# Kernel tuning notes

Hardware: AMD Instinct MI355X
Metric: run time of the kernel (lower is better)

Reference implementation:

```python
import jax, jax.numpy as jnp
import numpy as np

B, N, K = 4096, 64, 4


def _jump_sum(Ls, rho):
    # sum_k L_k @ rho @ L_k^dagger  (real dtype -> dagger == transpose)
    return jnp.einsum('kij,bjl,kml->bim', Ls, rho, Ls)


def _sandwich(U, rho):
    # U @ rho @ U^dagger
    return jnp.einsum('ij,bjl,ml->bim', U, rho, U)


def setup_inputs() -> dict:
    key = jax.random.key(0)
    k = jax.random.split(key, 6)
    eye = jnp.eye(N, dtype=jnp.float32)
    rho0 = jax.random.normal(k[0], (B, N, N), dtype=jnp.float32)
    # propagators: near-identity perturbations, Um well-conditioned for the LU solve
    U1 = eye + 0.1 * jax.random.normal(k[1], (N, N), dtype=jnp.float32)
    Um = eye + 0.1 * jax.random.normal(k[2], (N, N), dtype=jnp.float32)
    Ls0 = jax.random.normal(k[3], (K, N, N), dtype=jnp.float32)
    Lsmid = jax.random.normal(k[4], (K, N, N), dtype=jnp.float32)
    Ls1 = jax.random.normal(k[5], (K, N, N), dtype=jnp.float32)
    dt = jnp.asarray(0.01, dtype=jnp.float32)
    return {'rho0': rho0, 'U1': U1, 'Um': Um, 'Ls0': Ls0,
            'Lsmid': Lsmid, 'Ls1': Ls1, 'dt': dt}


def reference(rho0, U1, Um, Ls0, Lsmid, Ls1, dt):
    # propagator from t+dt/2 to t+dt via LU solve: solve(Um^T, U1^T)^T
    Um1 = jnp.linalg.solve(Um.T, U1.T).T

    # stage 1
    rho1 = rho0
    # stage 2 (SecondStage, no_jump_0 = Um, Ls = Ls0, aii = 0.5)
    rho2 = _sandwich(Um, rho0 + 0.5 * dt * _jump_sum(Ls0, rho1))
    # stage 3 (SameTimeStage, no_jump_0 = Um, Ls = Lsmid, aii = 0.5)
    rho3 = _sandwich(Um, rho0) + 0.5 * dt * _jump_sum(Lsmid, rho2)
    rho23 = rho2 + rho3
    # stage 4 (RKStage, no_jump_0 = U1, no_jump_i = Um1, Ls = Lsmid, aii = 1.0)
    rho4 = _sandwich(U1, rho0) + _sandwich(Um1, dt * _jump_sum(Lsmid, rho3))

    out = (_sandwich(U1, rho0 + (dt / 6) * _jump_sum(Ls0, rho1))
           + _sandwich(Um1, (dt / 3) * _jump_sum(Lsmid, rho23))
           + (dt / 6) * _jump_sum(Ls1, rho4))
    return out
```

## Files before the change

kernel.cpp:

```cpp
#include <hip/hip_runtime.h>


typedef __attribute__((ext_vector_type(16))) float f32x16;
typedef __attribute__((ext_vector_type(8))) __bf16 bf16x8;

#define MATB 8192

__device__ __forceinline__ unsigned short bf16rne(float x) {
  unsigned u = __builtin_bit_cast(unsigned, x);
  return (unsigned short)((u + 0x7FFFu + ((u >> 16) & 1u)) >> 16);
}
__device__ __forceinline__ float bflo(unsigned u) {
  return __builtin_bit_cast(float, u << 16);
}
__device__ __forceinline__ float bfhi(unsigned u) {
  return __builtin_bit_cast(float, u & 0xFFFF0000u);
}
__device__ __forceinline__ unsigned pk2(float lo, float hi) {
  union { __bf16 h[2]; unsigned u; } r;
  r.h[0] = (__bf16)lo;
  r.h[1] = (__bf16)hi;
  return r.u;
}

union U4 { uint4 u; bf16x8 h; };

__device__ __forceinline__ bf16x8 assemble(const f32x16& t, int b8, int lh) {
  unsigned u0 = pk2(t[b8 + 0], t[b8 + 1]);
  unsigned u1 = pk2(t[b8 + 2], t[b8 + 3]);
  unsigned w0 = pk2(t[b8 + 4], t[b8 + 5]);
  unsigned w1 = pk2(t[b8 + 6], t[b8 + 7]);
  unsigned z0 = lh ? u0 : w0;
  unsigned z1 = lh ? u1 : w1;
  unsigned r0 = __shfl_xor(z0, 32);
  unsigned r1 = __shfl_xor(z1, 32);
  U4 r;
  r.u = make_uint4(lh ? r0 : u0, lh ? r1 : u1,
                   lh ? w0 : r0, lh ? w1 : r1);
  return r.h;
}

__global__ __launch_bounds__(256) void kraus_invert(
    const float* __restrict__ U1, const float* __restrict__ Um,
    float* __restrict__ Um1) {
  __shared__ float M[64][66];
  __shared__ float X[64][66];
  int tid = threadIdx.x;
#pragma unroll
  for (int it = 0; it < 16; ++it) {
    int idx = tid + 256 * it;
    int r = idx >> 6, c = idx & 63;
    M[r][c] = Um[idx];
    X[r][c] = (r == c) ? 1.0f : 0.0f;
  }
  __syncthreads();
  for (int k = 0; k < 64; ++k) {
    if (tid < 64) {
      float ip = 1.0f / M[k][k];
      M[k][tid] *= ip;
      X[k][tid] *= ip;
    }
    __syncthreads();
    int r = tid & 63, q = tid >> 6;
    float f = M[r][k];
    __syncthreads();
    if (r != k) {
#pragma unroll
      for (int cc = 0; cc < 16; ++cc) {
        int c = q * 16 + cc;
        M[r][c] -= f * M[k][c];
        X[r][c] -= f * X[k][c];
      }
    }
    __syncthreads();
  }
  for (int it = 0; it < 16; ++it) {
    int idx = tid + 256 * it;
    int i = idx >> 6, j = idx & 63;
    float s = 0.0f;
#pragma unroll 4
    for (int k = 0; k < 64; ++k) s += U1[i * 64 + k] * X[k][j];
    Um1[idx] = s;
  }
}

__global__ __launch_bounds__(256) void kraus_prepack(
    const float* __restrict__ U1, const float* __restrict__ Um,
    const float* __restrict__ Ls0, const float* __restrict__ Lsmid,
    const float* __restrict__ Ls1, float* __restrict__ ws) {
  const float* Um1 = ws;
  unsigned short* dst = (unsigned short*)((char*)ws + 16384);
  int o = blockIdx.x;
  const float* s;
  if (o == 0) s = U1;
  else if (o == 1) s = Um;
  else if (o == 2) s = Um1;
  else if (o < 7) s = Ls0 + (o - 3) * 4096;
  else if (o < 11) s = Lsmid + (o - 7) * 4096;
  else s = Ls1 + (o - 11) * 4096;
  unsigned short* d = dst + o * 4096;
  int tid = threadIdx.x;
#pragma unroll
  for (int j = 0; j < 16; ++j) {
    int idx = tid + 256 * j;
    int f = idx >> 9, l = (idx >> 3) & 63, i = idx & 7;
    int t = f >> 2, ss = f & 3;
    int R = t * 32 + (l & 31);
    int C = ss * 16 + (l >> 5) * 8 + i;
    d[idx] = bf16rne(s[R * 64 + C]);
  }
}

__global__ __launch_bounds__(256, 4) void kraus_main(
    const float* __restrict__ rho0g, const float* __restrict__ dtp,
    const char* __restrict__ gfrag, float* __restrict__ outg) {
  __shared__ __align__(16) char lds[5 * MATB];
  char* S0 = lds;
  char* S1 = S0 + MATB;
  char* S2 = S1 + MATB;
  char* S3 = S2 + MATB;
  char* S4 = S3 + MATB;

  const int tid = threadIdx.x;
  const int l = tid & 63, w = tid >> 6;
  const int ti = w >> 1, tj = w & 1;
  const int l31 = l & 31, lh = l >> 5;
  const int fragoff = l * 16;
  const int myslot = ((tj * 4 + 2 * ti) << 10) + fragoff;
  const float dt = dtp[0];
  const size_t b = blockIdx.x;

  auto GF = [&](int op, int blk) {
    return gfrag + op * 8192 + blk * 4096 + l * 16;
  };
  auto mmA = [&](f32x16& acc, const char* X, int a, const char* __restrict__ gQ) {
#pragma unroll
    for (int s = 0; s < 4; ++s) {
      bf16x8 aa = *(const bf16x8*)(X + ((a * 4 + s) << 10) + fragoff);
      bf16x8 bb = *(const bf16x8*)(gQ + s * 1024);
      acc = __builtin_amdgcn_mfma_f32_32x32x16_bf16(aa, bb, acc, 0, 0, 0);
    }
  };
  auto sandP = [&](f32x16& acc, const char* X, int op1, int op2) {
    f32x16 t0 = {}, t1 = {};
    mmA(t0, X, 0, GF(op1, ti));
    mmA(t1, X, 1, GF(op1, ti));
    const char* gQ = GF(op2, tj);
#pragma unroll
    for (int s = 0; s < 4; ++s) {
      bf16x8 p = assemble((s < 2) ? t0 : t1, (s & 1) * 8, lh);
      bf16x8 q = *(const bf16x8*)(gQ + s * 1024);
      acc = __builtin_amdgcn_mfma_f32_32x32x16_bf16(p, q, acc, 0, 0, 0);
    }
  };
  auto storeF = [&](char* dst, const f32x16& acc) {
#pragma unroll
    for (int sg = 0; sg < 2; ++sg) {
      bf16x8 f = assemble(acc, sg * 8, lh);
      *(bf16x8*)(dst + myslot + (sg << 10)) = f;
    }
  };
  auto axpy = [&](char* D, const char* A, float s, const char* Bm) {
#pragma unroll
    for (int j = 0; j < 8; ++j) {
      int off = (tid + 256 * j) * 4;
      unsigned a = *(const unsigned*)(A + off);
      unsigned bb = *(const unsigned*)(Bm + off);
      *(unsigned*)(D + off) = pk2(bflo(a) + s * bflo(bb), bfhi(a) + s * bfhi(bb));
    }
  };

  {
    const float* src = rho0g + b * 4096 + tid * 16;
    float vals[16];
#pragma unroll
    for (int q = 0; q < 4; ++q) {
      float4 f = *(const float4*)(src + q * 4);
      vals[q * 4 + 0] = f.x; vals[q * 4 + 1] = f.y;
      vals[q * 4 + 2] = f.z; vals[q * 4 + 3] = f.w;
    }
    int r = tid >> 2, c0 = (tid & 3) * 16;
    int base = ((r >> 4) << 10) + ((r & 7) * 2) + (((r >> 3) & 1) * 32) * 16;
#pragma unroll
    for (int u = 0; u < 16; ++u) {
      int c = c0 + u;
      *(unsigned short*)(S0 + ((c >> 5) << 12) + base + (c & 31) * 16) =
          bf16rne(vals[u]);
    }
  }
  __syncthreads();

  f32x16 outacc = {};

  {
    f32x16 J = {};
#pragma unroll
    for (int k = 0; k < 4; ++k) sandP(J, S0, 3 + k, 3 + k);
    storeF(S1, J);
  }
  __syncthreads();

  {
    f32x16 a = {};
    sandP(a, S1, 0, 0);
    outacc += (dt / 6.f) * a;
    axpy(S2, S0, 0.5f * dt, S1);
  }
  __syncthreads();

  {
    { f32x16 A = {}; sandP(A, S0, 0, 0); outacc += A; storeF(S1, A); }
    { f32x16 r2 = {}; sandP(r2, S2, 1, 1); storeF(S3, r2); }
    { f32x16 Sh = {}; sandP(Sh, S0, 1, 1); storeF(S4, Sh); }
  }
  __syncthreads();

  {
    f32x16 J = {};
#pragma unroll
    for (int k = 0; k < 4; ++k) sandP(J, S3, 7 + k, 7 + k);
    storeF(S2, J);
  }
  __syncthreads();

  axpy(S3, S4, 0.5f * dt, S2);
  __syncthreads();

  {
    f32x16 J = {};
#pragma unroll
    for (int k = 0; k < 4; ++k) sandP(J, S3, 7 + k, 7 + k);
    storeF(S4, J);
  }
  __syncthreads();

  {
    { f32x16 a = {}; sandP(a, S2, 2, 2); outacc += (dt / 3.f) * a; }
    {
      f32x16 g = {};
      sandP(g, S4, 2, 2);
      outacc += (dt / 3.f) * g;
#pragma unroll
      for (int sg = 0; sg < 2; ++sg) {
        bf16x8 F = assemble(g, sg * 8, lh);
        char* p = S1 + myslot + (sg << 10);
        bf16x8 old = *(const bf16x8*)p;
        bf16x8 nw;
#pragma unroll
        for (int i = 0; i < 8; ++i)
          nw[i] = (__bf16)((float)old[i] + dt * (float)F[i]);
        *(bf16x8*)p = nw;
      }
    }
  }
  __syncthreads();

  {
    f32x16 J = {};
#pragma unroll
    for (int k = 0; k < 4; ++k) sandP(J, S1, 11 + k, 11 + k);
    outacc += (dt / 6.f) * J;
  }

  {
    float* op = outg + b * 4096 + (size_t)(ti * 32 + lh * 4) * 64 + tj * 32 + l31;
#pragma unroll
    for (int r = 0; r < 16; ++r) {
      int row = (r & 3) + 8 * (r >> 2);
      op[row * 64] = outacc[r];
    }
  }
}

extern "C" void kernel_launch(void* const* d_in, const int* in_sizes, int n_in,
                              void* d_out, int out_size, void* d_ws, size_t ws_size,
                              hipStream_t stream) {
  const float* rho0 = (const float*)d_in[0];
  const float* U1 = (const float*)d_in[1];
  const float* Um = (const float*)d_in[2];
  const float* Ls0 = (const float*)d_in[3];
  const float* Lsmid = (const float*)d_in[4];
  const float* Ls1 = (const float*)d_in[5];
  const float* dtp = (const float*)d_in[6];
  float* out = (float*)d_out;
  float* ws = (float*)d_ws;

  const int B = in_sizes[0] >> 12;

  kraus_invert<<<1, 256, 0, stream>>>(U1, Um, ws);
  kraus_prepack<<<15, 256, 0, stream>>>(U1, Um, Ls0, Lsmid, Ls1, ws);
  kraus_main<<<B, 256, 0, stream>>>(rho0, dtp, (const char*)d_ws + 16384, out);
}
```

Baseline: 284.8 us.

## Reuse LDS buffers to cut shared memory and fit five blocks per CU

Drops one of the five 8KB LDS staging buffers by reassigning buffer roles across stages. The rho0 buffer is overwritten in place by the Um sandwich result, with an extra barrier placed between the first-stage MMAs and the store. The launch bound rises from 4 to 5 blocks so more blocks can be resident per CU to hide latency. The tighter bound reduces the VGPR budget per thread, which risks register spills. The axpy indexing is also changed to give each wave a contiguous chunk of the buffer.

```diff
diff --git a/kernel.cpp b/kernel.cpp
--- a/kernel.cpp
+++ b/kernel.cpp
@@ -111,12 +111,11 @@
   }
 }
 
-__global__ __launch_bounds__(256, 4) void kraus_main(
+__global__ __launch_bounds__(256, 5) void kraus_main(
     const float* __restrict__ rho0g, const float* __restrict__ dtp,
     const char* __restrict__ gfrag, float* __restrict__ outg) {
-  __shared__ __align__(16) char lds[5 * MATB];
-  char* S0 = lds;
-  char* S1 = S0 + MATB;
+  __shared__ __align__(16) char lds[4 * MATB];
+  char* S1 = lds;
   char* S2 = S1 + MATB;
   char* S3 = S2 + MATB;
   char* S4 = S3 + MATB;
@@ -141,17 +140,20 @@
       acc = __builtin_amdgcn_mfma_f32_32x32x16_bf16(aa, bb, acc, 0, 0, 0);
     }
   };
+  auto second = [&](f32x16& acc, const f32x16& t0, const f32x16& t1,
+                    const char* __restrict__ gQ) {
+#pragma unroll
+    for (int s = 0; s < 4; ++s) {
+      bf16x8 p = assemble((s < 2) ? t0 : t1, (s & 1) * 8, lh);
+      bf16x8 q = *(const bf16x8*)(gQ + s * 1024);
+      acc = __builtin_amdgcn_mfma_f32_32x32x16_bf16(p, q, acc, 0, 0, 0);
+    }
+  };
   auto sandP = [&](f32x16& acc, const char* X, int op1, int op2) {
     f32x16 t0 = {}, t1 = {};
     mmA(t0, X, 0, GF(op1, ti));
     mmA(t1, X, 1, GF(op1, ti));
-    const char* gQ = GF(op2, tj);
-#pragma unroll
-    for (int s = 0; s < 4; ++s) {
-      bf16x8 p = assemble((s < 2) ? t0 : t1, (s & 1) * 8, lh);
-      bf16x8 q = *(const bf16x8*)(gQ + s * 1024);
-      acc = __builtin_amdgcn_mfma_f32_32x32x16_bf16(p, q, acc, 0, 0, 0);
-    }
+    second(acc, t0, t1, GF(op2, tj));
   };
   auto storeF = [&](char* dst, const f32x16& acc) {
 #pragma unroll
@@ -160,10 +162,10 @@
       *(bf16x8*)(dst + myslot + (sg << 10)) = f;
     }
   };
-  auto axpy = [&](char* D, const char* A, float s, const char* Bm) {
+  auto axpyQ = [&](char* D, const char* A, float s, const char* Bm) {
 #pragma unroll
     for (int j = 0; j < 8; ++j) {
-      int off = (tid + 256 * j) * 4;
+      int off = 2048 * w + (j * 64 + l) * 4;
       unsigned a = *(const unsigned*)(A + off);
       unsigned bb = *(const unsigned*)(Bm + off);
       *(unsigned*)(D + off) = pk2(bflo(a) + s * bflo(bb), bfhi(a) + s * bfhi(bb));
@@ -184,7 +186,7 @@
 #pragma unroll
     for (int u = 0; u < 16; ++u) {
       int c = c0 + u;
-      *(unsigned short*)(S0 + ((c >> 5) << 12) + base + (c & 31) * 16) =
+      *(unsigned short*)(S1 + ((c >> 5) << 12) + base + (c & 31) * 16) =
           bf16rne(vals[u]);
     }
   }
@@ -195,55 +197,63 @@
   {
     f32x16 J = {};
 #pragma unroll
-    for (int k = 0; k < 4; ++k) sandP(J, S0, 3 + k, 3 + k);
+    for (int k = 0; k < 4; ++k) sandP(J, S1, 3 + k, 3 + k);
+    storeF(S2, J);
+  }
+  __syncthreads();
+
+  {
+    f32x16 a = {};
+    sandP(a, S2, 0, 0);
+    outacc += (dt / 6.f) * a;
+    axpyQ(S3, S1, 0.5f * dt, S2);
+  }
+  __syncthreads();
+
+  {
+    { f32x16 A = {}; sandP(A, S1, 0, 0); outacc += A; storeF(S2, A); }
+    { f32x16 r2 = {}; sandP(r2, S3, 1, 1); storeF(S4, r2); }
+  }
+  {
+    f32x16 t0 = {}, t1 = {};
+    mmA(t0, S1, 0, GF(1, ti));
+    mmA(t1, S1, 1, GF(1, ti));
+    __syncthreads();
+    f32x16 a = {};
+    second(a, t0, t1, GF(1, tj));
+    storeF(S1, a);
+  }
+  __syncthreads();
+
+  {
+    f32x16 J = {};
+#pragma unroll
+    for (int k = 0; k < 4; ++k) sandP(J, S4, 7 + k, 7 + k);
+    storeF(S3, J);
+  }
+  __syncthreads();
+
+  axpyQ(S4, S1, 0.5f * dt, S3);
+  __syncthreads();
+
+  {
+    f32x16 J = {};
+#pragma unroll
+    for (int k = 0; k < 4; ++k) sandP(J, S4, 7 + k, 7 + k);
     storeF(S1, J);
   }
   __syncthreads();
 
   {
-    f32x16 a = {};
-    sandP(a, S1, 0, 0);
-    outacc += (dt / 6.f) * a;
-    axpy(S2, S0, 0.5f * dt, S1);
-  }
-  __syncthreads();
-
-  {
-    { f32x16 A = {}; sandP(A, S0, 0, 0); outacc += A; storeF(S1, A); }
-    { f32x16 r2 = {}; sandP(r2, S2, 1, 1); storeF(S3, r2); }
-    { f32x16 Sh = {}; sandP(Sh, S0, 1, 1); storeF(S4, Sh); }
-  }
-  __syncthreads();
-
-  {
-    f32x16 J = {};
-#pragma unroll
-    for (int k = 0; k < 4; ++k) sandP(J, S3, 7 + k, 7 + k);
-    storeF(S2, J);
-  }
-  __syncthreads();
-
-  axpy(S3, S4, 0.5f * dt, S2);
-  __syncthreads();
-
-  {
-    f32x16 J = {};
-#pragma unroll
-    for (int k = 0; k < 4; ++k) sandP(J, S3, 7 + k, 7 + k);
-    storeF(S4, J);
-  }
-  __syncthreads();
-
-  {
-    { f32x16 a = {}; sandP(a, S2, 2, 2); outacc += (dt / 3.f) * a; }
+    { f32x16 a = {}; sandP(a, S3, 2, 2); outacc += (dt / 3.f) * a; }
     {
       f32x16 g = {};
-      sandP(g, S4, 2, 2);
+      sandP(g, S1, 2, 2);
       outacc += (dt / 3.f) * g;
 #pragma unroll
       for (int sg = 0; sg < 2; ++sg) {
         bf16x8 F = assemble(g, sg * 8, lh);
-        char* p = S1 + myslot + (sg << 10);
+        char* p = S2 + myslot + (sg << 10);
         bf16x8 old = *(const bf16x8*)p;
         bf16x8 nw;
 #pragma unroll
@@ -258,7 +268,7 @@
   {
     f32x16 J = {};
 #pragma unroll
-    for (int k = 0; k < 4; ++k) sandP(J, S1, 11 + k, 11 + k);
+    for (int k = 0; k < 4; ++k) sandP(J, S2, 11 + k, 11 + k);
     outacc += (dt / 6.f) * J;
   }
 
```

New measurement: 417.9 us. +46.7%, slower.
